# Performance work log

Measured on AMD Instinct MI355X. Metric: run time of the kernel, lower is better.

Reference implementation:

```python
import jax, jax.numpy as jnp
import numpy as np

# ---- Instant-NGP 4D hash-grid constants (hard-coded in the torch module) ----
L = 16; F = 2; LOG2_T = 19; T = 1 << LOG2_T; N_MIN = 8; N_MAX = 2048
B_SCALE = np.exp(np.log(N_MAX / N_MIN) / (L - 1))
AABB = 1.0
PRIMES = np.array([1, 2654435761, 805459861, 3674351687], dtype=np.uint32)  # tcnn fast_hash primes (4D)
CORNERS = np.array([[(c >> d) & 1 for d in range(4)] for c in range(16)], dtype=np.int32)  # [16,4]


def _level_res(l):
    scale = np.exp2(l * np.log2(B_SCALE)) * N_MIN - 1.0  # tcnn grid_scale
    res = int(np.ceil(scale)) + 1
    return float(scale), res


def hash_encode(x, grid):
    """x: [N,4] in [0,1]; grid: [L,T,F]. Returns [N, L*F]."""
    feats = []
    for l in range(L):
        scale, res = _level_res(l)
        pos = x * scale + 0.5                      # tcnn position mapping
        g = jnp.floor(pos)
        frac = pos - g                             # [N,4]
        gi = g.astype(jnp.int32)
        corner = gi[:, None, :] + CORNERS[None]    # [N,16,4]
        w = jnp.prod(jnp.where(CORNERS[None].astype(bool), frac[:, None, :], 1.0 - frac[:, None, :]), axis=-1)  # [N,16]
        if res ** 4 <= T:
            # dense (stride) indexing for coarse levels, as tcnn does
            stride = jnp.array([1, res, res * res, res ** 3], dtype=jnp.int32)
            idx = jnp.minimum(jnp.sum(corner * stride, axis=-1), T - 1)
        else:
            cu = corner.astype(jnp.uint32)
            h = (cu[..., 0] * PRIMES[0]) ^ (cu[..., 1] * PRIMES[1]) ^ (cu[..., 2] * PRIMES[2]) ^ (cu[..., 3] * PRIMES[3])
            idx = (h & jnp.uint32(T - 1)).astype(jnp.int32)
        vals = grid[l][idx]                        # [N,16,F] irregular gather
        feats.append(jnp.sum(w[..., None] * vals, axis=1))  # quadrilinear interp -> [N,F]
    return jnp.concatenate(feats, axis=-1)         # [N,32]


def sh_deg4(d):
    """tcnn SphericalHarmonics degree 4; d in [-1,1]^3. Returns [N,16]."""
    x, y, z = d[:, 0], d[:, 1], d[:, 2]
    xy, xz, yz = x * y, x * z, y * z
    x2, y2, z2 = x * x, y * y, z * z
    return jnp.stack([
        jnp.full_like(x, 0.28209479177387814),
        -0.48860251190291987 * y,
        0.48860251190291987 * z,
        -0.48860251190291987 * x,
        1.0925484305920792 * xy,
        -1.0925484305920792 * yz,
        0.94617469575755997 * z2 - 0.31539156525251999,
        -1.0925484305920792 * xz,
        0.54627421529603959 * x2 - 0.54627421529603959 * y2,
        0.59004358992664352 * y * (-3.0 * x2 + y2),
        2.8906114426405538 * xy * z,
        0.45704579946446572 * y * (1.0 - 5.0 * z2),
        0.3731763325901154 * z * (5.0 * z2 - 3.0),
        0.45704579946446572 * x * (1.0 - 5.0 * z2),
        1.4453057213202769 * z * (x2 - y2),
        0.59004358992664352 * x * (-x2 + 3.0 * y2),
    ], axis=-1)


def setup_inputs() -> dict:
    key = jax.random.key(0)
    ks = jax.random.split(key, 8)
    N = 262144
    original_xyzs = jax.random.uniform(ks[0], (N, 4), dtype=jnp.float32)
    dirs = jax.random.uniform(ks[1], (N, 3), dtype=jnp.float32)
    # tcnn hash-grid init: uniform [-1e-4, 1e-4]
    grid = jax.random.uniform(ks[2], (L, T, F), dtype=jnp.float32, minval=-1e-4, maxval=1e-4)
    def he(k, o, i):
        return jax.random.normal(k, (o, i), dtype=jnp.float32) * np.sqrt(2.0 / i).astype(np.float32)
    W1 = he(ks[3], 64, 32)
    W2 = he(ks[4], 16, 64)
    Wc1 = he(ks[5], 64, 32)
    Wc2 = he(ks[6], 64, 64)
    Wc3 = he(ks[7], 3, 64)
    return {"original_xyzs": original_xyzs, "dirs": dirs, "grid": grid,
            "W1": W1, "W2": W2, "Wc1": Wc1, "Wc2": Wc2, "Wc3": Wc3}


def reference(original_xyzs, dirs, grid, W1, W2, Wc1, Wc2, Wc3):
    ts = original_xyzs[:, 3:4]
    xyz = (original_xyzs[:, :3] + AABB) / AABB / 2.0   # -> [0,1]
    inp = jnp.concatenate([xyz, ts], axis=1)           # [N,4]
    hr = hash_encode(inp, grid)                        # [N,32]
    # xyz_encoder: CutlassMLP 32->64 (ReLU) ->16, no biases
    h = jax.nn.relu(hr @ W1.T) @ W2.T                  # [N,16]
    sigma = jnp.exp(h[:, 0])                           # TruncExp forward
    sh = sh_deg4(dirs * 2.0 - 1.0)                     # [N,16]
    ci = jnp.concatenate([sh, h], axis=1)              # [N,32]
    color = jax.nn.sigmoid(jax.nn.relu(jax.nn.relu(ci @ Wc1.T) @ Wc2.T) @ Wc3.T)  # [N,3]
    return color, sigma
```

## Files before the change

kernel.cpp:

```cpp
#include <hip/hip_runtime.h>
#include <math.h>

#define THREADS 256
#define TMASK ((1u << 19) - 1u)

static __device__ __constant__ float kScale[16] = {
    7.0f,          10.57815398f,  15.75670563f,  23.25146503f,
    34.09839735f,  49.79683366f,  72.51669472f,  105.39843246f,
    152.98718950f, 221.86092960f, 321.53978800f, 465.80191600f,
    674.58804640f, 976.75780270f, 1414.07882380f, 2047.0f};
static __device__ __constant__ int kRes[4] = {8, 12, 17, 25};

__global__ void __launch_bounds__(THREADS, 6)
htrf_encode(const float* __restrict__ xyzs, const float* __restrict__ grid,
            float2* __restrict__ feat, int N, int CH, int H0) {
  const int b = blockIdx.x;
  const int x = b & 7;
  const int r = b >> 3;
  int level, chunk;
  if (r < CH) {
    level = 4 + x;
    chunk = r;
  } else {
    const int j = r - CH;
    level = 12 + (x >> 1);
    chunk = (x & 1) ? (H0 + j) : j;
    if (chunk >= CH) return;
  }
  const int tid = threadIdx.x;
  const int wave = tid >> 6;
  const int lane = tid & 63;
  const int p_local = lane >> 4;
  const int c = lane & 15;
  const int cx = c & 1, cy = (c >> 1) & 1, cz = (c >> 2) & 1, ct = (c >> 3) & 1;

  const int base = chunk * THREADS + wave * 64;
  const int gp = base + lane;
  float4 pre = make_float4(0.f, 0.f, 0.f, 0.f);
  if (gp < N) pre = reinterpret_cast<const float4*>(xyzs)[gp];

  const float s = kScale[level];
  const float2* __restrict__ gl =
      reinterpret_cast<const float2*>(grid) + ((size_t)level << 19);

  #pragma unroll 4
  for (int it = 0; it < 16; ++it) {
    const int src = it * 4 + p_local;
    const float q0 = (__shfl(pre.x, src, 64) + 1.0f) * 0.5f;
    const float q1 = (__shfl(pre.y, src, 64) + 1.0f) * 0.5f;
    const float q2 = (__shfl(pre.z, src, 64) + 1.0f) * 0.5f;
    const float q3 = __shfl(pre.w, src, 64);

    const float pos0 = fmaf(q0, s, 0.5f);
    const float pos1 = fmaf(q1, s, 0.5f);
    const float pos2 = fmaf(q2, s, 0.5f);
    const float pos3 = fmaf(q3, s, 0.5f);
    const float fl0 = floorf(pos0), fl1 = floorf(pos1);
    const float fl2 = floorf(pos2), fl3 = floorf(pos3);
    const float f0 = pos0 - fl0, f1 = pos1 - fl1;
    const float f2 = pos2 - fl2, f3 = pos3 - fl3;
    const int g0 = (int)fl0, g1 = (int)fl1, g2 = (int)fl2, g3 = (int)fl3;

    const unsigned ux = (unsigned)(g0 + cx);
    const unsigned uy = (unsigned)(g1 + cy) * 2654435761u;
    const unsigned uz = (unsigned)(g2 + cz) * 805459861u;
    const unsigned ut = (unsigned)(g3 + ct) * 3674351687u;
    const unsigned idx = (ux ^ uy ^ uz ^ ut) & TMASK;

    const float w = (cx ? f0 : 1.0f - f0) * (cy ? f1 : 1.0f - f1) *
                    (cz ? f2 : 1.0f - f2) * (ct ? f3 : 1.0f - f3);

    const float2 v = gl[idx];
    float s0 = w * v.x;
    float s1 = w * v.y;
    s0 += __shfl_xor(s0, 1, 64);  s1 += __shfl_xor(s1, 1, 64);
    s0 += __shfl_xor(s0, 2, 64);  s1 += __shfl_xor(s1, 2, 64);
    s0 += __shfl_xor(s0, 4, 64);  s1 += __shfl_xor(s1, 4, 64);
    s0 += __shfl_xor(s0, 8, 64);  s1 += __shfl_xor(s1, 8, 64);

    const int n = base + it * 4 + p_local;
    if (c == 0 && n < N) feat[(size_t)(level - 4) * N + n] = make_float2(s0, s1);
  }
}

__global__ void __launch_bounds__(THREADS, 4)
htrf_mlp1(const float* __restrict__ xyzs, const float* __restrict__ grid,
          const float* __restrict__ W1, const float* __restrict__ W2,
          float* __restrict__ ws, float* __restrict__ out, int N) {
  const int n = blockIdx.x * THREADS + threadIdx.x;
  if (n >= N) return;

  const float4 p = reinterpret_cast<const float4*>(xyzs)[n];
  const float q0 = (p.x + 1.0f) * 0.5f;
  const float q1 = (p.y + 1.0f) * 0.5f;
  const float q2 = (p.z + 1.0f) * 0.5f;
  const float q3 = p.w;

  float fr[32];
  #pragma unroll
  for (int l = 0; l < 4; ++l) {
    const float s = kScale[l];
    const float pos0 = fmaf(q0, s, 0.5f);
    const float pos1 = fmaf(q1, s, 0.5f);
    const float pos2 = fmaf(q2, s, 0.5f);
    const float pos3 = fmaf(q3, s, 0.5f);
    const float fl0 = floorf(pos0), fl1 = floorf(pos1);
    const float fl2 = floorf(pos2), fl3 = floorf(pos3);
    const float f0 = pos0 - fl0, f1 = pos1 - fl1;
    const float f2 = pos2 - fl2, f3 = pos3 - fl3;
    const int g0 = (int)fl0, g1 = (int)fl1, g2 = (int)fl2, g3 = (int)fl3;

    float wxy[4], wzt[4];
    {
      const float u0 = 1.0f - f0, u1 = 1.0f - f1, u2 = 1.0f - f2, u3 = 1.0f - f3;
      wxy[0] = u0 * u1; wxy[1] = f0 * u1; wxy[2] = u0 * f1; wxy[3] = f0 * f1;
      wzt[0] = u2 * u3; wzt[1] = f2 * u3; wzt[2] = u2 * f3; wzt[3] = f2 * f3;
    }
    const int rr = kRes[l];
    const int r2 = rr * rr, r3 = r2 * rr;
    const int sxy[4] = {g0 + g1 * rr, g0 + 1 + g1 * rr,
                        g0 + (g1 + 1) * rr, g0 + 1 + (g1 + 1) * rr};
    const int szt[4] = {g2 * r2 + g3 * r3, (g2 + 1) * r2 + g3 * r3,
                        g2 * r2 + (g3 + 1) * r3, (g2 + 1) * r2 + (g3 + 1) * r3};
    const float2* __restrict__ gl =
        reinterpret_cast<const float2*>(grid) + ((size_t)l << 19);
    float2 vv[16];
    #pragma unroll
    for (int cc = 0; cc < 16; ++cc) {
      const int v = sxy[cc & 3] + szt[cc >> 2];
      const int idx = v < (int)TMASK ? v : (int)TMASK;
      vv[cc] = gl[idx];
    }
    float a0 = 0.0f, a1 = 0.0f;
    #pragma unroll
    for (int cc = 0; cc < 16; ++cc) {
      const float w = wxy[cc & 3] * wzt[cc >> 2];
      a0 = fmaf(w, vv[cc].x, a0);
      a1 = fmaf(w, vv[cc].y, a1);
    }
    fr[2 * l] = a0;
    fr[2 * l + 1] = a1;
  }
  const float2* __restrict__ feat = reinterpret_cast<const float2*>(ws);
  #pragma unroll
  for (int l = 0; l < 12; ++l) {
    const float2 v = feat[(size_t)l * N + n];
    fr[8 + 2 * l] = v.x;
    fr[9 + 2 * l] = v.y;
  }

  float h[16];
  #pragma unroll
  for (int i = 0; i < 16; ++i) h[i] = 0.0f;

  #pragma unroll 1
  for (int j = 0; j < 64; ++j) {
    const float* __restrict__ w = W1 + j * 32;
    float b0 = 0.f, b1 = 0.f, b2 = 0.f, b3 = 0.f;
    #pragma unroll
    for (int k = 0; k < 32; k += 4) {
      b0 = fmaf(fr[k + 0], w[k + 0], b0);
      b1 = fmaf(fr[k + 1], w[k + 1], b1);
      b2 = fmaf(fr[k + 2], w[k + 2], b2);
      b3 = fmaf(fr[k + 3], w[k + 3], b3);
    }
    const float act = fmaxf((b0 + b1) + (b2 + b3), 0.0f);
    #pragma unroll
    for (int i = 0; i < 16; ++i) h[i] = fmaf(act, W2[i * 64 + j], h[i]);
  }
  out[3 * N + n] = expf(h[0]);
  #pragma unroll
  for (int i = 0; i < 16; ++i) ws[(size_t)i * N + n] = h[i];
}

__global__ void __launch_bounds__(THREADS, 3)
htrf_color(const float* __restrict__ dirs, const float* __restrict__ Wc1,
           const float* __restrict__ Wc2, const float* __restrict__ Wc3,
           const float* __restrict__ ws, float* __restrict__ out, int N) {
  const int n = blockIdx.x * THREADS + threadIdx.x;
  if (n >= N) return;

  const float dxr = dirs[3 * n + 0], dyr = dirs[3 * n + 1], dzr = dirs[3 * n + 2];
  const float x = fmaf(dxr, 2.0f, -1.0f);
  const float y = fmaf(dyr, 2.0f, -1.0f);
  const float z = fmaf(dzr, 2.0f, -1.0f);
  const float xy = x * y, xz = x * z, yz = y * z;
  const float x2 = x * x, y2 = y * y, z2 = z * z;
  float ci[32];
  ci[0]  = 0.28209479177387814f;
  ci[1]  = -0.48860251190291987f * y;
  ci[2]  = 0.48860251190291987f * z;
  ci[3]  = -0.48860251190291987f * x;
  ci[4]  = 1.0925484305920792f * xy;
  ci[5]  = -1.0925484305920792f * yz;
  ci[6]  = 0.94617469575756f * z2 - 0.31539156525252f;
  ci[7]  = -1.0925484305920792f * xz;
  ci[8]  = 0.5462742152960396f * x2 - 0.5462742152960396f * y2;
  ci[9]  = 0.5900435899266435f * y * (-3.0f * x2 + y2);
  ci[10] = 2.890611442640554f * xy * z;
  ci[11] = 0.4570457994644657f * y * (1.0f - 5.0f * z2);
  ci[12] = 0.3731763325901154f * z * (5.0f * z2 - 3.0f);
  ci[13] = 0.4570457994644657f * x * (1.0f - 5.0f * z2);
  ci[14] = 1.445305721320277f * z * (x2 - y2);
  ci[15] = 0.5900435899266435f * x * (-x2 + 3.0f * y2);
  #pragma unroll
  for (int i = 0; i < 16; ++i) ci[16 + i] = ws[(size_t)i * N + n];

  float c2p[64];
  #pragma unroll
  for (int i = 0; i < 64; ++i) c2p[i] = 0.0f;

  #pragma unroll 1
  for (int j = 0; j < 64; ++j) {
    const float* __restrict__ w = Wc1 + j * 32;
    float b0 = 0.f, b1 = 0.f, b2 = 0.f, b3 = 0.f;
    #pragma unroll
    for (int k = 0; k < 32; k += 4) {
      b0 = fmaf(ci[k + 0], w[k + 0], b0);
      b1 = fmaf(ci[k + 1], w[k + 1], b1);
      b2 = fmaf(ci[k + 2], w[k + 2], b2);
      b3 = fmaf(ci[k + 3], w[k + 3], b3);
    }
    const float act = fmaxf((b0 + b1) + (b2 + b3), 0.0f);
    #pragma unroll
    for (int i = 0; i < 64; ++i) c2p[i] = fmaf(act, Wc2[i * 64 + j], c2p[i]);
  }

  float l0a = 0.f, l0b = 0.f, l1a = 0.f, l1b = 0.f, l2a = 0.f, l2b = 0.f;
  #pragma unroll
  for (int i = 0; i < 64; i += 2) {
    const float a0r = fmaxf(c2p[i], 0.0f);
    const float a1r = fmaxf(c2p[i + 1], 0.0f);
    l0a = fmaf(a0r, Wc3[0 * 64 + i], l0a);
    l0b = fmaf(a1r, Wc3[0 * 64 + i + 1], l0b);
    l1a = fmaf(a0r, Wc3[1 * 64 + i], l1a);
    l1b = fmaf(a1r, Wc3[1 * 64 + i + 1], l1b);
    l2a = fmaf(a0r, Wc3[2 * 64 + i], l2a);
    l2b = fmaf(a1r, Wc3[2 * 64 + i + 1], l2b);
  }
  out[3 * n + 0] = 1.0f / (1.0f + expf(-(l0a + l0b)));
  out[3 * n + 1] = 1.0f / (1.0f + expf(-(l1a + l1b)));
  out[3 * n + 2] = 1.0f / (1.0f + expf(-(l2a + l2b)));
}

__global__ void __launch_bounds__(THREADS)
htrf_fused(const float* __restrict__ xyzs, const float* __restrict__ dirs,
           const float* __restrict__ grid, const float* __restrict__ W1,
           const float* __restrict__ W2, const float* __restrict__ Wc1,
           const float* __restrict__ Wc2, const float* __restrict__ Wc3,
           float* __restrict__ out, int N) {
  __shared__ float sbuf[THREADS * 33];
  const int tid = threadIdx.x;
  const int n = blockIdx.x * THREADS + tid;
  if (n >= N) return;
  float* __restrict__ my = sbuf + tid * 33;

  const float4 p = reinterpret_cast<const float4*>(xyzs)[n];
  const float q0 = (p.x + 1.0f) * 0.5f;
  const float q1 = (p.y + 1.0f) * 0.5f;
  const float q2 = (p.z + 1.0f) * 0.5f;
  const float q3 = p.w;

  #pragma unroll 1
  for (int l = 0; l < 16; ++l) {
    const float s = kScale[l];
    const float pos0 = fmaf(q0, s, 0.5f);
    const float pos1 = fmaf(q1, s, 0.5f);
    const float pos2 = fmaf(q2, s, 0.5f);
    const float pos3 = fmaf(q3, s, 0.5f);
    const float fl0 = floorf(pos0), fl1 = floorf(pos1);
    const float fl2 = floorf(pos2), fl3 = floorf(pos3);
    const float f0 = pos0 - fl0, f1 = pos1 - fl1;
    const float f2 = pos2 - fl2, f3 = pos3 - fl3;
    const int g0 = (int)fl0, g1 = (int)fl1, g2 = (int)fl2, g3 = (int)fl3;

    float wxy[4], wzt[4];
    {
      const float u0 = 1.0f - f0, u1 = 1.0f - f1, u2 = 1.0f - f2, u3 = 1.0f - f3;
      wxy[0] = u0 * u1; wxy[1] = f0 * u1; wxy[2] = u0 * f1; wxy[3] = f0 * f1;
      wzt[0] = u2 * u3; wzt[1] = f2 * u3; wzt[2] = u2 * f3; wzt[3] = f2 * f3;
    }

    unsigned idx[16];
    if (l < 4) {
      const int rr = kRes[l];
      const int r2 = rr * rr, r3 = r2 * rr;
      const int sxy[4] = {g0 + g1 * rr, g0 + 1 + g1 * rr,
                          g0 + (g1 + 1) * rr, g0 + 1 + (g1 + 1) * rr};
      const int szt[4] = {g2 * r2 + g3 * r3, (g2 + 1) * r2 + g3 * r3,
                          g2 * r2 + (g3 + 1) * r3, (g2 + 1) * r2 + (g3 + 1) * r3};
      #pragma unroll
      for (int cc = 0; cc < 16; ++cc) {
        const int v = sxy[cc & 3] + szt[cc >> 2];
        idx[cc] = (unsigned)(v < (int)TMASK ? v : (int)TMASK);
      }
    } else {
      const unsigned hx0 = (unsigned)g0,               hx1 = (unsigned)(g0 + 1);
      const unsigned hy0 = (unsigned)g1 * 2654435761u, hy1 = (unsigned)(g1 + 1) * 2654435761u;
      const unsigned hz0 = (unsigned)g2 * 805459861u,  hz1 = (unsigned)(g2 + 1) * 805459861u;
      const unsigned ht0 = (unsigned)g3 * 3674351687u, ht1 = (unsigned)(g3 + 1) * 3674351687u;
      const unsigned sxy[4] = {hx0 ^ hy0, hx1 ^ hy0, hx0 ^ hy1, hx1 ^ hy1};
      const unsigned szt[4] = {hz0 ^ ht0, hz1 ^ ht0, hz0 ^ ht1, hz1 ^ ht1};
      #pragma unroll
      for (int cc = 0; cc < 16; ++cc)
        idx[cc] = (sxy[cc & 3] ^ szt[cc >> 2]) & TMASK;
    }

    const float2* __restrict__ gl =
        reinterpret_cast<const float2*>(grid) + ((size_t)l << 19);
    float2 vv[16];
    #pragma unroll
    for (int cc = 0; cc < 16; ++cc) vv[cc] = gl[idx[cc]];
    float a0 = 0.0f, a1 = 0.0f;
    #pragma unroll
    for (int cc = 0; cc < 16; ++cc) {
      const float w = wxy[cc & 3] * wzt[cc >> 2];
      a0 = fmaf(w, vv[cc].x, a0);
      a1 = fmaf(w, vv[cc].y, a1);
    }
    my[2 * l] = a0;
    my[2 * l + 1] = a1;
  }

  float fr[32];
  #pragma unroll
  for (int k = 0; k < 32; ++k) fr[k] = my[k];

  float h[16];
  #pragma unroll
  for (int i = 0; i < 16; ++i) h[i] = 0.0f;

  #pragma unroll 1
  for (int j = 0; j < 64; ++j) {
    const float* __restrict__ w = W1 + j * 32;
    float b0 = 0.f, b1 = 0.f, b2 = 0.f, b3 = 0.f;
    #pragma unroll
    for (int k = 0; k < 32; k += 4) {
      b0 = fmaf(fr[k + 0], w[k + 0], b0);
      b1 = fmaf(fr[k + 1], w[k + 1], b1);
      b2 = fmaf(fr[k + 2], w[k + 2], b2);
      b3 = fmaf(fr[k + 3], w[k + 3], b3);
    }
    const float act = fmaxf((b0 + b1) + (b2 + b3), 0.0f);
    #pragma unroll
    for (int i = 0; i < 16; ++i) h[i] = fmaf(act, W2[i * 64 + j], h[i]);
  }
  const float sigma = expf(h[0]);

  const float dxr = dirs[3 * n + 0], dyr = dirs[3 * n + 1], dzr = dirs[3 * n + 2];
  const float x = fmaf(dxr, 2.0f, -1.0f);
  const float y = fmaf(dyr, 2.0f, -1.0f);
  const float z = fmaf(dzr, 2.0f, -1.0f);
  const float xy = x * y, xz = x * z, yz = y * z;
  const float x2 = x * x, y2 = y * y, z2 = z * z;
  float ci[32];
  ci[0]  = 0.28209479177387814f;
  ci[1]  = -0.48860251190291987f * y;
  ci[2]  = 0.48860251190291987f * z;
  ci[3]  = -0.48860251190291987f * x;
  ci[4]  = 1.0925484305920792f * xy;
  ci[5]  = -1.0925484305920792f * yz;
  ci[6]  = 0.94617469575756f * z2 - 0.31539156525252f;
  ci[7]  = -1.0925484305920792f * xz;
  ci[8]  = 0.5462742152960396f * x2 - 0.5462742152960396f * y2;
  ci[9]  = 0.5900435899266435f * y * (-3.0f * x2 + y2);
  ci[10] = 2.890611442640554f * xy * z;
  ci[11] = 0.4570457994644657f * y * (1.0f - 5.0f * z2);
  ci[12] = 0.3731763325901154f * z * (5.0f * z2 - 3.0f);
  ci[13] = 0.4570457994644657f * x * (1.0f - 5.0f * z2);
  ci[14] = 1.445305721320277f * z * (x2 - y2);
  ci[15] = 0.5900435899266435f * x * (-x2 + 3.0f * y2);
  #pragma unroll
  for (int i = 0; i < 16; ++i) ci[16 + i] = h[i];

  float c2p[64];
  #pragma unroll
  for (int i = 0; i < 64; ++i) c2p[i] = 0.0f;

  #pragma unroll 1
  for (int j = 0; j < 64; ++j) {
    const float* __restrict__ w = Wc1 + j * 32;
    float b0 = 0.f, b1 = 0.f, b2 = 0.f, b3 = 0.f;
    #pragma unroll
    for (int k = 0; k < 32; k += 4) {
      b0 = fmaf(ci[k + 0], w[k + 0], b0);
      b1 = fmaf(ci[k + 1], w[k + 1], b1);
      b2 = fmaf(ci[k + 2], w[k + 2], b2);
      b3 = fmaf(ci[k + 3], w[k + 3], b3);
    }
    const float act = fmaxf((b0 + b1) + (b2 + b3), 0.0f);
    #pragma unroll
    for (int i = 0; i < 64; ++i) c2p[i] = fmaf(act, Wc2[i * 64 + j], c2p[i]);
  }

  float l0a = 0.f, l0b = 0.f, l1a = 0.f, l1b = 0.f, l2a = 0.f, l2b = 0.f;
  #pragma unroll
  for (int i = 0; i < 64; i += 2) {
    const float a0r = fmaxf(c2p[i], 0.0f);
    const float a1r = fmaxf(c2p[i + 1], 0.0f);
    l0a = fmaf(a0r, Wc3[0 * 64 + i], l0a);
    l0b = fmaf(a1r, Wc3[0 * 64 + i + 1], l0b);
    l1a = fmaf(a0r, Wc3[1 * 64 + i], l1a);
    l1b = fmaf(a1r, Wc3[1 * 64 + i + 1], l1b);
    l2a = fmaf(a0r, Wc3[2 * 64 + i], l2a);
    l2b = fmaf(a1r, Wc3[2 * 64 + i + 1], l2b);
  }
  out[3 * n + 0] = 1.0f / (1.0f + expf(-(l0a + l0b)));
  out[3 * n + 1] = 1.0f / (1.0f + expf(-(l1a + l1b)));
  out[3 * n + 2] = 1.0f / (1.0f + expf(-(l2a + l2b)));
  out[3 * N + n] = sigma;
}

extern "C" void kernel_launch(void* const* d_in, const int* in_sizes, int n_in,
                              void* d_out, int out_size, void* d_ws, size_t ws_size,
                              hipStream_t stream) {
  const int N = in_sizes[0] / 4;
  const size_t need = (size_t)12 * (size_t)N * sizeof(float2);
  if (ws_size >= need) {
    const int CH = (N + THREADS - 1) / THREADS;
    const int H0 = (CH + 1) / 2;
    const int NB = 8 * (CH + H0);
    const int PB = (N + THREADS - 1) / THREADS;
    htrf_encode<<<dim3(NB), dim3(THREADS), 0, stream>>>(
        (const float*)d_in[0], (const float*)d_in[2], (float2*)d_ws, N, CH, H0);
    htrf_mlp1<<<dim3(PB), dim3(THREADS), 0, stream>>>(
        (const float*)d_in[0], (const float*)d_in[2], (const float*)d_in[3],
        (const float*)d_in[4], (float*)d_ws, (float*)d_out, N);
    htrf_color<<<dim3(PB), dim3(THREADS), 0, stream>>>(
        (const float*)d_in[1], (const float*)d_in[5], (const float*)d_in[6],
        (const float*)d_in[7], (const float*)d_ws, (float*)d_out, N);
  } else {
    htrf_fused<<<dim3((N + THREADS - 1) / THREADS), dim3(THREADS), 0, stream>>>(
        (const float*)d_in[0], (const float*)d_in[1], (const float*)d_in[2],
        (const float*)d_in[3], (const float*)d_in[4], (const float*)d_in[5],
        (const float*)d_in[6], (const float*)d_in[7], (float*)d_out, N);
  }
}
```

Baseline: 370.8 us.

## Fuse MLP stages into one bf16 MFMA kernel and coalesce encode stores

Replaces the separate scalar-FMA density MLP and color MLP kernels with one kernel that runs all four layers as bf16 16x16x32 MFMAs, staging activations in LDS per wave. This removes the workspace round trip of the 16 hidden features between kernels and moves the dense matmul work from VALU to matrix cores. The hash-encode kernel now gathers each point's result into its own lane with shuffles so every lane stores once, coalesced, instead of one lane per 16 writing. Rounding weights and activations to bf16 reduces precision, and the large LDS footprint may limit occupancy.

```diff
diff --git a/kernel.cpp b/kernel.cpp
--- a/kernel.cpp
+++ b/kernel.cpp
@@ -3,6 +3,9 @@
 
 #define THREADS 256
 #define TMASK ((1u << 19) - 1u)
+
+typedef __attribute__((ext_vector_type(8))) short short8;
+typedef __attribute__((ext_vector_type(4))) float f32x4;
 
 static __device__ __constant__ float kScale[16] = {
     7.0f,          10.57815398f,  15.75670563f,  23.25146503f,
@@ -10,6 +13,12 @@
     152.98718950f, 221.86092960f, 321.53978800f, 465.80191600f,
     674.58804640f, 976.75780270f, 1414.07882380f, 2047.0f};
 static __device__ __constant__ int kRes[4] = {8, 12, 17, 25};
+
+static __device__ __forceinline__ unsigned short f2bf(float f) {
+  unsigned u = __builtin_bit_cast(unsigned, f);
+  unsigned r = u + 0x7FFFu + ((u >> 16) & 1u);
+  return (unsigned short)(r >> 16);
+}
 
 __global__ void __launch_bounds__(THREADS, 6)
 htrf_encode(const float* __restrict__ xyzs, const float* __restrict__ grid,
@@ -43,6 +52,7 @@
   const float2* __restrict__ gl =
       reinterpret_cast<const float2*>(grid) + ((size_t)level << 19);
 
+  float r0 = 0.0f, r1 = 0.0f;
   #pragma unroll 4
   for (int it = 0; it < 16; ++it) {
     const int src = it * 4 + p_local;
@@ -77,18 +87,270 @@
     s0 += __shfl_xor(s0, 2, 64);  s1 += __shfl_xor(s1, 2, 64);
     s0 += __shfl_xor(s0, 4, 64);  s1 += __shfl_xor(s1, 4, 64);
     s0 += __shfl_xor(s0, 8, 64);  s1 += __shfl_xor(s1, 8, 64);
-
-    const int n = base + it * 4 + p_local;
-    if (c == 0 && n < N) feat[(size_t)(level - 4) * N + n] = make_float2(s0, s1);
-  }
+    const float t0 = __shfl(s0, (lane & 3) << 4, 64);
+    const float t1 = __shfl(s1, (lane & 3) << 4, 64);
+    if ((lane >> 2) == it) { r0 = t0; r1 = t1; }
+  }
+  if (gp < N) feat[(size_t)(level - 4) * N + gp] = make_float2(r0, r1);
 }
 
-__global__ void __launch_bounds__(THREADS, 4)
-htrf_mlp1(const float* __restrict__ xyzs, const float* __restrict__ grid,
-          const float* __restrict__ W1, const float* __restrict__ W2,
-          float* __restrict__ ws, float* __restrict__ out, int N) {
-  const int n = blockIdx.x * THREADS + threadIdx.x;
+__global__ void __launch_bounds__(THREADS, 3)
+htrf_mlp_mfma(const float* __restrict__ xyzs, const float* __restrict__ dirs,
+              const float* __restrict__ grid, const float* __restrict__ W1,
+              const float* __restrict__ W2, const float* __restrict__ Wc1,
+              const float* __restrict__ Wc2, const float* __restrict__ Wc3,
+              const float2* __restrict__ feat, float* __restrict__ out, int N) {
+  __shared__ unsigned short Xs[256 * 40];
+  __shared__ unsigned short CIs[256 * 40];
+  __shared__ unsigned short ACTs[4][16 * 72];
+  __shared__ float W3s[192];
+
+  const int tid = threadIdx.x;
+  const int lane = tid & 63;
+  const int wv = tid >> 6;
+  const int m = lane & 15;
+  const int ks = lane >> 4;
+  const int n = blockIdx.x * THREADS + tid;
+
+  short8 w1f[4], wc1f[4], w2f[2], wc2f[4][2];
+  #pragma unroll
+  for (int t = 0; t < 4; ++t) {
+    const float4 a = *reinterpret_cast<const float4*>(W1 + (t * 16 + m) * 32 + ks * 8);
+    const float4 bq = *reinterpret_cast<const float4*>(W1 + (t * 16 + m) * 32 + ks * 8 + 4);
+    short8 sv;
+    sv[0]=(short)f2bf(a.x); sv[1]=(short)f2bf(a.y); sv[2]=(short)f2bf(a.z); sv[3]=(short)f2bf(a.w);
+    sv[4]=(short)f2bf(bq.x); sv[5]=(short)f2bf(bq.y); sv[6]=(short)f2bf(bq.z); sv[7]=(short)f2bf(bq.w);
+    w1f[t] = sv;
+  }
+  #pragma unroll
+  for (int t = 0; t < 4; ++t) {
+    const float4 a = *reinterpret_cast<const float4*>(Wc1 + (t * 16 + m) * 32 + ks * 8);
+    const float4 bq = *reinterpret_cast<const float4*>(Wc1 + (t * 16 + m) * 32 + ks * 8 + 4);
+    short8 sv;
+    sv[0]=(short)f2bf(a.x); sv[1]=(short)f2bf(a.y); sv[2]=(short)f2bf(a.z); sv[3]=(short)f2bf(a.w);
+    sv[4]=(short)f2bf(bq.x); sv[5]=(short)f2bf(bq.y); sv[6]=(short)f2bf(bq.z); sv[7]=(short)f2bf(bq.w);
+    wc1f[t] = sv;
+  }
+  #pragma unroll
+  for (int kk = 0; kk < 2; ++kk) {
+    const float4 a = *reinterpret_cast<const float4*>(W2 + m * 64 + kk * 32 + ks * 8);
+    const float4 bq = *reinterpret_cast<const float4*>(W2 + m * 64 + kk * 32 + ks * 8 + 4);
+    short8 sv;
+    sv[0]=(short)f2bf(a.x); sv[1]=(short)f2bf(a.y); sv[2]=(short)f2bf(a.z); sv[3]=(short)f2bf(a.w);
+    sv[4]=(short)f2bf(bq.x); sv[5]=(short)f2bf(bq.y); sv[6]=(short)f2bf(bq.z); sv[7]=(short)f2bf(bq.w);
+    w2f[kk] = sv;
+  }
+  #pragma unroll
+  for (int t = 0; t < 4; ++t)
+    #pragma unroll
+    for (int kk = 0; kk < 2; ++kk) {
+      const float4 a = *reinterpret_cast<const float4*>(Wc2 + (t * 16 + m) * 64 + kk * 32 + ks * 8);
+      const float4 bq = *reinterpret_cast<const float4*>(Wc2 + (t * 16 + m) * 64 + kk * 32 + ks * 8 + 4);
+      short8 sv;
+      sv[0]=(short)f2bf(a.x); sv[1]=(short)f2bf(a.y); sv[2]=(short)f2bf(a.z); sv[3]=(short)f2bf(a.w);
+      sv[4]=(short)f2bf(bq.x); sv[5]=(short)f2bf(bq.y); sv[6]=(short)f2bf(bq.z); sv[7]=(short)f2bf(bq.w);
+      wc2f[t][kk] = sv;
+    }
+  if (tid < 192) W3s[tid] = Wc3[tid];
+
+  if (n < N) {
+    const float4 p = reinterpret_cast<const float4*>(xyzs)[n];
+    const float q0 = (p.x + 1.0f) * 0.5f;
+    const float q1 = (p.y + 1.0f) * 0.5f;
+    const float q2 = (p.z + 1.0f) * 0.5f;
+    const float q3 = p.w;
+
+    float fr[32];
+    #pragma unroll
+    for (int l = 0; l < 4; ++l) {
+      const float s = kScale[l];
+      const float pos0 = fmaf(q0, s, 0.5f);
+      const float pos1 = fmaf(q1, s, 0.5f);
+      const float pos2 = fmaf(q2, s, 0.5f);
+      const float pos3 = fmaf(q3, s, 0.5f);
+      const float fl0 = floorf(pos0), fl1 = floorf(pos1);
+      const float fl2 = floorf(pos2), fl3 = floorf(pos3);
+      const float f0 = pos0 - fl0, f1 = pos1 - fl1;
+      const float f2 = pos2 - fl2, f3 = pos3 - fl3;
+      const int g0 = (int)fl0, g1 = (int)fl1, g2 = (int)fl2, g3 = (int)fl3;
+
+      float wxy[4], wzt[4];
+      {
+        const float u0 = 1.0f - f0, u1 = 1.0f - f1, u2 = 1.0f - f2, u3 = 1.0f - f3;
+        wxy[0] = u0 * u1; wxy[1] = f0 * u1; wxy[2] = u0 * f1; wxy[3] = f0 * f1;
+        wzt[0] = u2 * u3; wzt[1] = f2 * u3; wzt[2] = u2 * f3; wzt[3] = f2 * f3;
+      }
+      const int rr = kRes[l];
+      const int r2 = rr * rr, r3 = r2 * rr;
+      const int sxy[4] = {g0 + g1 * rr, g0 + 1 + g1 * rr,
+                          g0 + (g1 + 1) * rr, g0 + 1 + (g1 + 1) * rr};
+      const int szt[4] = {g2 * r2 + g3 * r3, (g2 + 1) * r2 + g3 * r3,
+                          g2 * r2 + (g3 + 1) * r3, (g2 + 1) * r2 + (g3 + 1) * r3};
+      const float2* __restrict__ gld =
+          reinterpret_cast<const float2*>(grid) + ((size_t)l << 19);
+      float2 vv[16];
+      #pragma unroll
+      for (int cc = 0; cc < 16; ++cc) {
+        const int v = sxy[cc & 3] + szt[cc >> 2];
+        const int idx = v < (int)TMASK ? v : (int)TMASK;
+        vv[cc] = gld[idx];
+      }
+      float a0 = 0.0f, a1 = 0.0f;
+      #pragma unroll
+      for (int cc = 0; cc < 16; ++cc) {
+        const float w = wxy[cc & 3] * wzt[cc >> 2];
+        a0 = fmaf(w, vv[cc].x, a0);
+        a1 = fmaf(w, vv[cc].y, a1);
+      }
+      fr[2 * l] = a0;
+      fr[2 * l + 1] = a1;
+    }
+    #pragma unroll
+    for (int l = 0; l < 12; ++l) {
+      const float2 v = feat[(size_t)l * N + n];
+      fr[8 + 2 * l] = v.x;
+      fr[9 + 2 * l] = v.y;
+    }
+    #pragma unroll
+    for (int g = 0; g < 4; ++g) {
+      short8 sv;
+      #pragma unroll
+      for (int i = 0; i < 8; ++i) sv[i] = (short)f2bf(fr[g * 8 + i]);
+      *reinterpret_cast<short8*>(&Xs[tid * 40 + g * 8]) = sv;
+    }
+
+    const float dxr = dirs[3 * n + 0], dyr = dirs[3 * n + 1], dzr = dirs[3 * n + 2];
+    const float x = fmaf(dxr, 2.0f, -1.0f);
+    const float y = fmaf(dyr, 2.0f, -1.0f);
+    const float z = fmaf(dzr, 2.0f, -1.0f);
+    const float xy = x * y, xz = x * z, yz = y * z;
+    const float x2 = x * x, y2 = y * y, z2 = z * z;
+    float sh[16];
+    sh[0]  = 0.28209479177387814f;
+    sh[1]  = -0.48860251190291987f * y;
+    sh[2]  = 0.48860251190291987f * z;
+    sh[3]  = -0.48860251190291987f * x;
+    sh[4]  = 1.0925484305920792f * xy;
+    sh[5]  = -1.0925484305920792f * yz;
+    sh[6]  = 0.94617469575756f * z2 - 0.31539156525252f;
+    sh[7]  = -1.0925484305920792f * xz;
+    sh[8]  = 0.5462742152960396f * x2 - 0.5462742152960396f * y2;
+    sh[9]  = 0.5900435899266435f * y * (-3.0f * x2 + y2);
+    sh[10] = 2.890611442640554f * xy * z;
+    sh[11] = 0.4570457994644657f * y * (1.0f - 5.0f * z2);
+    sh[12] = 0.3731763325901154f * z * (5.0f * z2 - 3.0f);
+    sh[13] = 0.4570457994644657f * x * (1.0f - 5.0f * z2);
+    sh[14] = 1.445305721320277f * z * (x2 - y2);
+    sh[15] = 0.5900435899266435f * x * (-x2 + 3.0f * y2);
+    #pragma unroll
+    for (int g = 0; g < 2; ++g) {
+      short8 sv;
+      #pragma unroll
+      for (int i = 0; i < 8; ++i) sv[i] = (short)f2bf(sh[g * 8 + i]);
+      *reinterpret_cast<short8*>(&CIs[tid * 40 + g * 8]) = sv;
+    }
+  }
+  __syncthreads();
+
+  unsigned short* __restrict__ act = &ACTs[wv][0];
+  #pragma unroll 1
+  for (int tt = 0; tt < 4; ++tt) {
+    const int tb = wv * 64 + tt * 16;
+    const size_t gpt = (size_t)blockIdx.x * 256 + tb;
+    const short8 a1 = *reinterpret_cast<const short8*>(&Xs[(tb + m) * 40 + ks * 8]);
+    #pragma unroll
+    for (int t = 0; t < 4; ++t) {
+      f32x4 z = {0.f, 0.f, 0.f, 0.f};
+      const f32x4 d = __builtin_amdgcn_mfma_f32_16x16x32_bf16(a1, w1f[t], z, 0, 0, 0);
+      #pragma unroll
+      for (int rr = 0; rr < 4; ++rr)
+        act[(ks * 4 + rr) * 72 + t * 16 + m] = f2bf(fmaxf(d[rr], 0.0f));
+    }
+    {
+      const short8 a2k0 = *reinterpret_cast<const short8*>(&act[m * 72 + ks * 8]);
+      const short8 a2k1 = *reinterpret_cast<const short8*>(&act[m * 72 + 32 + ks * 8]);
+      f32x4 dh = {0.f, 0.f, 0.f, 0.f};
+      dh = __builtin_amdgcn_mfma_f32_16x16x32_bf16(a2k0, w2f[0], dh, 0, 0, 0);
+      dh = __builtin_amdgcn_mfma_f32_16x16x32_bf16(a2k1, w2f[1], dh, 0, 0, 0);
+      #pragma unroll
+      for (int rr = 0; rr < 4; ++rr) {
+        const size_t pt = gpt + ks * 4 + rr;
+        if (m == 0 && pt < (size_t)N) out[3 * (size_t)N + pt] = expf(dh[rr]);
+        CIs[(tb + ks * 4 + rr) * 40 + 16 + m] = f2bf(dh[rr]);
+      }
+    }
+    const short8 a3 = *reinterpret_cast<const short8*>(&CIs[(tb + m) * 40 + ks * 8]);
+    #pragma unroll
+    for (int t = 0; t < 4; ++t) {
+      f32x4 z = {0.f, 0.f, 0.f, 0.f};
+      const f32x4 d = __builtin_amdgcn_mfma_f32_16x16x32_bf16(a3, wc1f[t], z, 0, 0, 0);
+      #pragma unroll
+      for (int rr = 0; rr < 4; ++rr)
+        act[(ks * 4 + rr) * 72 + t * 16 + m] = f2bf(fmaxf(d[rr], 0.0f));
+    }
+    f32x4 e0, e1, e2, e3;
+    {
+      const short8 a4k0 = *reinterpret_cast<const short8*>(&act[m * 72 + ks * 8]);
+      const short8 a4k1 = *reinterpret_cast<const short8*>(&act[m * 72 + 32 + ks * 8]);
+      f32x4 z = {0.f, 0.f, 0.f, 0.f};
+      e0 = __builtin_amdgcn_mfma_f32_16x16x32_bf16(a4k0, wc2f[0][0], z, 0, 0, 0);
+      e0 = __builtin_amdgcn_mfma_f32_16x16x32_bf16(a4k1, wc2f[0][1], e0, 0, 0, 0);
+      e1 = __builtin_amdgcn_mfma_f32_16x16x32_bf16(a4k0, wc2f[1][0], z, 0, 0, 0);
+      e1 = __builtin_amdgcn_mfma_f32_16x16x32_bf16(a4k1, wc2f[1][1], e1, 0, 0, 0);
+      e2 = __builtin_amdgcn_mfma_f32_16x16x32_bf16(a4k0, wc2f[2][0], z, 0, 0, 0);
+      e2 = __builtin_amdgcn_mfma_f32_16x16x32_bf16(a4k1, wc2f[2][1], e2, 0, 0, 0);
+      e3 = __builtin_amdgcn_mfma_f32_16x16x32_bf16(a4k0, wc2f[3][0], z, 0, 0, 0);
+      e3 = __builtin_amdgcn_mfma_f32_16x16x32_bf16(a4k1, wc2f[3][1], e3, 0, 0, 0);
+    }
+    float lg0[4], lg1[4], lg2[4];
+    {
+      const float w00 = W3s[0 * 64 + 0 * 16 + m], w01 = W3s[0 * 64 + 1 * 16 + m],
+                  w02 = W3s[0 * 64 + 2 * 16 + m], w03 = W3s[0 * 64 + 3 * 16 + m];
+      const float w10 = W3s[1 * 64 + 0 * 16 + m], w11 = W3s[1 * 64 + 1 * 16 + m],
+                  w12 = W3s[1 * 64 + 2 * 16 + m], w13 = W3s[1 * 64 + 3 * 16 + m];
+      const float w20 = W3s[2 * 64 + 0 * 16 + m], w21 = W3s[2 * 64 + 1 * 16 + m],
+                  w22 = W3s[2 * 64 + 2 * 16 + m], w23 = W3s[2 * 64 + 3 * 16 + m];
+      #pragma unroll
+      for (int rr = 0; rr < 4; ++rr) {
+        const float v0 = fmaxf(e0[rr], 0.0f), v1 = fmaxf(e1[rr], 0.0f);
+        const float v2 = fmaxf(e2[rr], 0.0f), v3 = fmaxf(e3[rr], 0.0f);
+        lg0[rr] = fmaf(v0, w00, fmaf(v1, w01, fmaf(v2, w02, v3 * w03)));
+        lg1[rr] = fmaf(v0, w10, fmaf(v1, w11, fmaf(v2, w12, v3 * w13)));
+        lg2[rr] = fmaf(v0, w20, fmaf(v1, w21, fmaf(v2, w22, v3 * w23)));
+      }
+    }
+    #pragma unroll
+    for (int st = 1; st < 16; st <<= 1) {
+      #pragma unroll
+      for (int rr = 0; rr < 4; ++rr) {
+        lg0[rr] += __shfl_xor(lg0[rr], st, 64);
+        lg1[rr] += __shfl_xor(lg1[rr], st, 64);
+        lg2[rr] += __shfl_xor(lg2[rr], st, 64);
+      }
+    }
+    #pragma unroll
+    for (int rr = 0; rr < 4; ++rr) {
+      const size_t pt = gpt + ks * 4 + rr;
+      if (pt < (size_t)N) {
+        if (m == 0) out[3 * pt + 0] = 1.0f / (1.0f + expf(-lg0[rr]));
+        if (m == 1) out[3 * pt + 1] = 1.0f / (1.0f + expf(-lg1[rr]));
+        if (m == 2) out[3 * pt + 2] = 1.0f / (1.0f + expf(-lg2[rr]));
+      }
+    }
+  }
+}
+
+__global__ void __launch_bounds__(THREADS)
+htrf_fused(const float* __restrict__ xyzs, const float* __restrict__ dirs,
+           const float* __restrict__ grid, const float* __restrict__ W1,
+           const float* __restrict__ W2, const float* __restrict__ Wc1,
+           const float* __restrict__ Wc2, const float* __restrict__ Wc3,
+           float* __restrict__ out, int N) {
+  __shared__ float sbuf[THREADS * 33];
+  const int tid = threadIdx.x;
+  const int n = blockIdx.x * THREADS + tid;
   if (n >= N) return;
+  float* __restrict__ my = sbuf + tid * 33;
 
   const float4 p = reinterpret_cast<const float4*>(xyzs)[n];
   const float q0 = (p.x + 1.0f) * 0.5f;
@@ -96,9 +358,8 @@
   const float q2 = (p.z + 1.0f) * 0.5f;
   const float q3 = p.w;
 
-  float fr[32];
-  #pragma unroll
-  for (int l = 0; l < 4; ++l) {
+  #pragma unroll 1
+  for (int l = 0; l < 16; ++l) {
     const float s = kScale[l];
     const float pos0 = fmaf(q0, s, 0.5f);
     const float pos1 = fmaf(q1, s, 0.5f);
@@ -116,21 +377,37 @@
       wxy[0] = u0 * u1; wxy[1] = f0 * u1; wxy[2] = u0 * f1; wxy[3] = f0 * f1;
       wzt[0] = u2 * u3; wzt[1] = f2 * u3; wzt[2] = u2 * f3; wzt[3] = f2 * f3;
     }
-    const int rr = kRes[l];
-    const int r2 = rr * rr, r3 = r2 * rr;
-    const int sxy[4] = {g0 + g1 * rr, g0 + 1 + g1 * rr,
-                        g0 + (g1 + 1) * rr, g0 + 1 + (g1 + 1) * rr};
-    const int szt[4] = {g2 * r2 + g3 * r3, (g2 + 1) * r2 + g3 * r3,
-                        g2 * r2 + (g3 + 1) * r3, (g2 + 1) * r2 + (g3 + 1) * r3};
+
+    unsigned idx[16];
+    if (l < 4) {
+      const int rr = kRes[l];
+      const int r2 = rr * rr, r3 = r2 * rr;
+      const int sxy[4] = {g0 + g1 * rr, g0 + 1 + g1 * rr,
+                          g0 + (g1 + 1) * rr, g0 + 1 + (g1 + 1) * rr};
+      const int szt[4] = {g2 * r2 + g3 * r3, (g2 + 1) * r2 + g3 * r3,
+                          g2 * r2 + (g3 + 1) * r3, (g2 + 1) * r2 + (g3 + 1) * r3};
+      #pragma unroll
+      for (int cc = 0; cc < 16; ++cc) {
+        const int v = sxy[cc & 3] + szt[cc >> 2];
+        idx[cc] = (unsigned)(v < (int)TMASK ? v : (int)TMASK);
+      }
+    } else {
+      const unsigned hx0 = (unsigned)g0,               hx1 = (unsigned)(g0 + 1);
+      const unsigned hy0 = (unsigned)g1 * 2654435761u, hy1 = (unsigned)(g1 + 1) * 2654435761u;
+      const unsigned hz0 = (unsigned)g2 * 805459861u,  hz1 = (unsigned)(g2 + 1) * 805459861u;
+      const unsigned ht0 = (unsigned)g3 * 3674351687u, ht1 = (unsigned)(g3 + 1) * 3674351687u;
+      const unsigned sxy[4] = {hx0 ^ hy0, hx1 ^ hy0, hx0 ^ hy1, hx1 ^ hy1};
+      const unsigned szt[4] = {hz0 ^ ht0, hz1 ^ ht0, hz0 ^ ht1, hz1 ^ ht1};
+      #pragma unroll
+      for (int cc = 0; cc < 16; ++cc)
+        idx[cc] = (sxy[cc & 3] ^ szt[cc >> 2]) & TMASK;
+    }
+
     const float2* __restrict__ gl =
         reinterpret_cast<const float2*>(grid) + ((size_t)l << 19);
     float2 vv[16];
     #pragma unroll
-    for (int cc = 0; cc < 16; ++cc) {
-      const int v = sxy[cc & 3] + szt[cc >> 2];
-      const int idx = v < (int)TMASK ? v : (int)TMASK;
-      vv[cc] = gl[idx];
-    }
+    for (int cc = 0; cc < 16; ++cc) vv[cc] = gl[idx[cc]];
     float a0 = 0.0f, a1 = 0.0f;
     #pragma unroll
     for (int cc = 0; cc < 16; ++cc) {
@@ -138,16 +415,13 @@
       a0 = fmaf(w, vv[cc].x, a0);
       a1 = fmaf(w, vv[cc].y, a1);
     }
-    fr[2 * l] = a0;
-    fr[2 * l + 1] = a1;
-  }
-  const float2* __restrict__ feat = reinterpret_cast<const float2*>(ws);
-  #pragma unroll
-  for (int l = 0; l < 12; ++l) {
-    const float2 v = feat[(size_t)l * N + n];
-    fr[8 + 2 * l] = v.x;
-    fr[9 + 2 * l] = v.y;
-  }
+    my[2 * l] = a0;
+    my[2 * l + 1] = a1;
+  }
+
+  float fr[32];
+  #pragma unroll
+  for (int k = 0; k < 32; ++k) fr[k] = my[k];
 
   float h[16];
   #pragma unroll
@@ -168,17 +442,7 @@
     #pragma unroll
     for (int i = 0; i < 16; ++i) h[i] = fmaf(act, W2[i * 64 + j], h[i]);
   }
-  out[3 * N + n] = expf(h[0]);
-  #pragma unroll
-  for (int i = 0; i < 16; ++i) ws[(size_t)i * N + n] = h[i];
-}
-
-__global__ void __launch_bounds__(THREADS, 3)
-htrf_color(const float* __restrict__ dirs, const float* __restrict__ Wc1,
-           const float* __restrict__ Wc2, const float* __restrict__ Wc3,
-           const float* __restrict__ ws, float* __restrict__ out, int N) {
-  const int n = blockIdx.x * THREADS + threadIdx.x;
-  if (n >= N) return;
+  const float sigma = expf(h[0]);
 
   const float dxr = dirs[3 * n + 0], dyr = dirs[3 * n + 1], dzr = dirs[3 * n + 2];
   const float x = fmaf(dxr, 2.0f, -1.0f);
@@ -204,173 +468,6 @@
   ci[14] = 1.445305721320277f * z * (x2 - y2);
   ci[15] = 0.5900435899266435f * x * (-x2 + 3.0f * y2);
   #pragma unroll
-  for (int i = 0; i < 16; ++i) ci[16 + i] = ws[(size_t)i * N + n];
-
-  float c2p[64];
-  #pragma unroll
-  for (int i = 0; i < 64; ++i) c2p[i] = 0.0f;
-
-  #pragma unroll 1
-  for (int j = 0; j < 64; ++j) {
-    const float* __restrict__ w = Wc1 + j * 32;
-    float b0 = 0.f, b1 = 0.f, b2 = 0.f, b3 = 0.f;
-    #pragma unroll
-    for (int k = 0; k < 32; k += 4) {
-      b0 = fmaf(ci[k + 0], w[k + 0], b0);
-      b1 = fmaf(ci[k + 1], w[k + 1], b1);
-      b2 = fmaf(ci[k + 2], w[k + 2], b2);
-      b3 = fmaf(ci[k + 3], w[k + 3], b3);
-    }
-    const float act = fmaxf((b0 + b1) + (b2 + b3), 0.0f);
-    #pragma unroll
-    for (int i = 0; i < 64; ++i) c2p[i] = fmaf(act, Wc2[i * 64 + j], c2p[i]);
-  }
-
-  float l0a = 0.f, l0b = 0.f, l1a = 0.f, l1b = 0.f, l2a = 0.f, l2b = 0.f;
-  #pragma unroll
-  for (int i = 0; i < 64; i += 2) {
-    const float a0r = fmaxf(c2p[i], 0.0f);
-    const float a1r = fmaxf(c2p[i + 1], 0.0f);
-    l0a = fmaf(a0r, Wc3[0 * 64 + i], l0a);
-    l0b = fmaf(a1r, Wc3[0 * 64 + i + 1], l0b);
-    l1a = fmaf(a0r, Wc3[1 * 64 + i], l1a);
-    l1b = fmaf(a1r, Wc3[1 * 64 + i + 1], l1b);
-    l2a = fmaf(a0r, Wc3[2 * 64 + i], l2a);
-    l2b = fmaf(a1r, Wc3[2 * 64 + i + 1], l2b);
-  }
-  out[3 * n + 0] = 1.0f / (1.0f + expf(-(l0a + l0b)));
-  out[3 * n + 1] = 1.0f / (1.0f + expf(-(l1a + l1b)));
-  out[3 * n + 2] = 1.0f / (1.0f + expf(-(l2a + l2b)));
-}
-
-__global__ void __launch_bounds__(THREADS)
-htrf_fused(const float* __restrict__ xyzs, const float* __restrict__ dirs,
-           const float* __restrict__ grid, const float* __restrict__ W1,
-           const float* __restrict__ W2, const float* __restrict__ Wc1,
-           const float* __restrict__ Wc2, const float* __restrict__ Wc3,
-           float* __restrict__ out, int N) {
-  __shared__ float sbuf[THREADS * 33];
-  const int tid = threadIdx.x;
-  const int n = blockIdx.x * THREADS + tid;
-  if (n >= N) return;
-  float* __restrict__ my = sbuf + tid * 33;
-
-  const float4 p = reinterpret_cast<const float4*>(xyzs)[n];
-  const float q0 = (p.x + 1.0f) * 0.5f;
-  const float q1 = (p.y + 1.0f) * 0.5f;
-  const float q2 = (p.z + 1.0f) * 0.5f;
-  const float q3 = p.w;
-
-  #pragma unroll 1
-  for (int l = 0; l < 16; ++l) {
-    const float s = kScale[l];
-    const float pos0 = fmaf(q0, s, 0.5f);
-    const float pos1 = fmaf(q1, s, 0.5f);
-    const float pos2 = fmaf(q2, s, 0.5f);
-    const float pos3 = fmaf(q3, s, 0.5f);
-    const float fl0 = floorf(pos0), fl1 = floorf(pos1);
-    const float fl2 = floorf(pos2), fl3 = floorf(pos3);
-    const float f0 = pos0 - fl0, f1 = pos1 - fl1;
-    const float f2 = pos2 - fl2, f3 = pos3 - fl3;
-    const int g0 = (int)fl0, g1 = (int)fl1, g2 = (int)fl2, g3 = (int)fl3;
-
-    float wxy[4], wzt[4];
-    {
-      const float u0 = 1.0f - f0, u1 = 1.0f - f1, u2 = 1.0f - f2, u3 = 1.0f - f3;
-      wxy[0] = u0 * u1; wxy[1] = f0 * u1; wxy[2] = u0 * f1; wxy[3] = f0 * f1;
-      wzt[0] = u2 * u3; wzt[1] = f2 * u3; wzt[2] = u2 * f3; wzt[3] = f2 * f3;
-    }
-
-    unsigned idx[16];
-    if (l < 4) {
-      const int rr = kRes[l];
-      const int r2 = rr * rr, r3 = r2 * rr;
-      const int sxy[4] = {g0 + g1 * rr, g0 + 1 + g1 * rr,
-                          g0 + (g1 + 1) * rr, g0 + 1 + (g1 + 1) * rr};
-      const int szt[4] = {g2 * r2 + g3 * r3, (g2 + 1) * r2 + g3 * r3,
-                          g2 * r2 + (g3 + 1) * r3, (g2 + 1) * r2 + (g3 + 1) * r3};
-      #pragma unroll
-      for (int cc = 0; cc < 16; ++cc) {
-        const int v = sxy[cc & 3] + szt[cc >> 2];
-        idx[cc] = (unsigned)(v < (int)TMASK ? v : (int)TMASK);
-      }
-    } else {
-      const unsigned hx0 = (unsigned)g0,               hx1 = (unsigned)(g0 + 1);
-      const unsigned hy0 = (unsigned)g1 * 2654435761u, hy1 = (unsigned)(g1 + 1) * 2654435761u;
-      const unsigned hz0 = (unsigned)g2 * 805459861u,  hz1 = (unsigned)(g2 + 1) * 805459861u;
-      const unsigned ht0 = (unsigned)g3 * 3674351687u, ht1 = (unsigned)(g3 + 1) * 3674351687u;
-      const unsigned sxy[4] = {hx0 ^ hy0, hx1 ^ hy0, hx0 ^ hy1, hx1 ^ hy1};
-      const unsigned szt[4] = {hz0 ^ ht0, hz1 ^ ht0, hz0 ^ ht1, hz1 ^ ht1};
-      #pragma unroll
-      for (int cc = 0; cc < 16; ++cc)
-        idx[cc] = (sxy[cc & 3] ^ szt[cc >> 2]) & TMASK;
-    }
-
-    const float2* __restrict__ gl =
-        reinterpret_cast<const float2*>(grid) + ((size_t)l << 19);
-    float2 vv[16];
-    #pragma unroll
-    for (int cc = 0; cc < 16; ++cc) vv[cc] = gl[idx[cc]];
-    float a0 = 0.0f, a1 = 0.0f;
-    #pragma unroll
-    for (int cc = 0; cc < 16; ++cc) {
-      const float w = wxy[cc & 3] * wzt[cc >> 2];
-      a0 = fmaf(w, vv[cc].x, a0);
-      a1 = fmaf(w, vv[cc].y, a1);
-    }
-    my[2 * l] = a0;
-    my[2 * l + 1] = a1;
-  }
-
-  float fr[32];
-  #pragma unroll
-  for (int k = 0; k < 32; ++k) fr[k] = my[k];
-
-  float h[16];
-  #pragma unroll
-  for (int i = 0; i < 16; ++i) h[i] = 0.0f;
-
-  #pragma unroll 1
-  for (int j = 0; j < 64; ++j) {
-    const float* __restrict__ w = W1 + j * 32;
-    float b0 = 0.f, b1 = 0.f, b2 = 0.f, b3 = 0.f;
-    #pragma unroll
-    for (int k = 0; k < 32; k += 4) {
-      b0 = fmaf(fr[k + 0], w[k + 0], b0);
-      b1 = fmaf(fr[k + 1], w[k + 1], b1);
-      b2 = fmaf(fr[k + 2], w[k + 2], b2);
-      b3 = fmaf(fr[k + 3], w[k + 3], b3);
-    }
-    const float act = fmaxf((b0 + b1) + (b2 + b3), 0.0f);
-    #pragma unroll
-    for (int i = 0; i < 16; ++i) h[i] = fmaf(act, W2[i * 64 + j], h[i]);
-  }
-  const float sigma = expf(h[0]);
-
-  const float dxr = dirs[3 * n + 0], dyr = dirs[3 * n + 1], dzr = dirs[3 * n + 2];
-  const float x = fmaf(dxr, 2.0f, -1.0f);
-  const float y = fmaf(dyr, 2.0f, -1.0f);
-  const float z = fmaf(dzr, 2.0f, -1.0f);
-  const float xy = x * y, xz = x * z, yz = y * z;
-  const float x2 = x * x, y2 = y * y, z2 = z * z;
-  float ci[32];
-  ci[0]  = 0.28209479177387814f;
-  ci[1]  = -0.48860251190291987f * y;
-  ci[2]  = 0.48860251190291987f * z;
-  ci[3]  = -0.48860251190291987f * x;
-  ci[4]  = 1.0925484305920792f * xy;
-  ci[5]  = -1.0925484305920792f * yz;
-  ci[6]  = 0.94617469575756f * z2 - 0.31539156525252f;
-  ci[7]  = -1.0925484305920792f * xz;
-  ci[8]  = 0.5462742152960396f * x2 - 0.5462742152960396f * y2;
-  ci[9]  = 0.5900435899266435f * y * (-3.0f * x2 + y2);
-  ci[10] = 2.890611442640554f * xy * z;
-  ci[11] = 0.4570457994644657f * y * (1.0f - 5.0f * z2);
-  ci[12] = 0.3731763325901154f * z * (5.0f * z2 - 3.0f);
-  ci[13] = 0.4570457994644657f * x * (1.0f - 5.0f * z2);
-  ci[14] = 1.445305721320277f * z * (x2 - y2);
-  ci[15] = 0.5900435899266435f * x * (-x2 + 3.0f * y2);
-  #pragma unroll
   for (int i = 0; i < 16; ++i) ci[16 + i] = h[i];
 
   float c2p[64];
@@ -423,12 +520,11 @@
     const int PB = (N + THREADS - 1) / THREADS;
     htrf_encode<<<dim3(NB), dim3(THREADS), 0, stream>>>(
         (const float*)d_in[0], (const float*)d_in[2], (float2*)d_ws, N, CH, H0);
-    htrf_mlp1<<<dim3(PB), dim3(THREADS), 0, stream>>>(
-        (const float*)d_in[0], (const float*)d_in[2], (const float*)d_in[3],
-        (const float*)d_in[4], (float*)d_ws, (float*)d_out, N);
-    htrf_color<<<dim3(PB), dim3(THREADS), 0, stream>>>(
-        (const float*)d_in[1], (const float*)d_in[5], (const float*)d_in[6],
-        (const float*)d_in[7], (const float*)d_ws, (float*)d_out, N);
+    htrf_mlp_mfma<<<dim3(PB), dim3(THREADS), 0, stream>>>(
+        (const float*)d_in[0], (const float*)d_in[1], (const float*)d_in[2],
+        (const float*)d_in[3], (const float*)d_in[4], (const float*)d_in[5],
+        (const float*)d_in[6], (const float*)d_in[7], (const float2*)d_ws,
+        (float*)d_out, N);
   } else {
     htrf_fused<<<dim3((N + THREADS - 1) / THREADS), dim3(THREADS), 0, stream>>>(
         (const float*)d_in[0], (const float*)d_in[1], (const float*)d_in[2],
```

Measured after the change: 354.1 us. -4.5%, faster.
